# Performance work log

Measured on AMD Instinct MI355X. Metric: run time of the kernel, lower is better.

Reference implementation:

```python
import jax, jax.numpy as jnp
import numpy as np

# 2^22-point radix-2 DIT FFT; NOTE the original code applies tf.abs at EVERY
# recursion level (not just the top), so each butterfly stage is followed by a
# magnitude + recomplexification. We reproduce that exact (non-standard) math.
N = 1 << 22
STAGES = 22


def _bitrev_perm(n, bits):
    # vectorized bit-reversal permutation (the order induced by the even/odd
    # decimation inputs[0::2] / inputs[1::2] recursion)
    x = np.arange(n)
    r = np.zeros(n, dtype=np.int64)
    for b in range(bits):
        r = (r << 1) | ((x >> b) & 1)
    return r


_PERM = jnp.asarray(_bitrev_perm(N, STAGES))


def setup_inputs() -> dict:
    key = jax.random.key(0)
    x = jax.random.normal(key, (N,), dtype=jnp.float32)
    return {"x": x}


def reference(x):
    # base case of the recursion: length-1 leaves are the bit-reversed inputs
    y = x[_PERM].astype(jnp.complex64)
    for s in range(1, STAGES + 1):  # fixed log2(N) stages, not a data loop
        m = 1 << s                  # sub-FFT size at this stage
        yb = y.reshape(N // m, m)   # [num_blocks, m]
        e = yb[:, : m // 2]         # 'even' sub-results
        o = yb[:, m // 2:]          # 'odd'  sub-results
        # twiddles W(m, k) = exp(-2*pi*i*k/m)
        tw = jnp.exp(
            jnp.complex64(-2j * np.pi) * jnp.arange(m // 2, dtype=jnp.float32) / m
        ).astype(jnp.complex64)
        t = tw[None, :] * o
        # butterfly then tf.abs (applied at every level in the original)
        mag = jnp.abs(jnp.concatenate([e + t, e - t], axis=1)).reshape(N)
        y = mag.astype(jnp.complex64) if s < STAGES else mag
    return y  # float32 magnitudes, shape [N]
```

## Files before the change

### kernel.cpp

```cpp
#include <hip/hip_runtime.h>
#include <math.h>


#define NBITS 22
#define RSQ2 0.70710678118654752440f

__device__ __forceinline__ float hsqrt(float x) { return __builtin_amdgcn_sqrtf(x); }

__device__ __forceinline__ void bf(float& e, float& o, float c, float s) {
    float rp = fmaf(c, o, e);
    float rm = fmaf(-c, o, e);
    float im = s * o;
    float im2 = im * im;
    e = hsqrt(fmaf(rp, rp, im2));
    o = hsqrt(fmaf(rm, rm, im2));
}
__device__ __forceinline__ void bf0(float& e, float& o) {
    float a = e + o, b = e - o;
    e = fabsf(a); o = fabsf(b);
}
__device__ __forceinline__ void bfq(float& e, float& o) {
    float h = hsqrt(fmaf(e, e, o * o));
    e = h; o = h;
}

__device__ __forceinline__ void radix8f(float v[8], float c2, float s2) {
    float c1 = fmaf(-2.f * s2, s2, 1.f);
    float s1 = 2.f * s2 * c2;
    float c0 = fmaf(-2.f * s1, s1, 1.f);
    float s0 = 2.f * s1 * c1;
    bf(v[0], v[1], c0, s0); bf(v[2], v[3], c0, s0);
    bf(v[4], v[5], c0, s0); bf(v[6], v[7], c0, s0);
    bf(v[0], v[2], c1, s1); bf(v[4], v[6], c1, s1);
    bf(v[1], v[3], -s1, c1); bf(v[5], v[7], -s1, c1);
    bf(v[0], v[4], c2, s2);
    float u = RSQ2 * (c2 - s2), w = RSQ2 * (c2 + s2);
    bf(v[1], v[5], u, w);
    bf(v[2], v[6], -s2, c2);
    bf(v[3], v[7], -w, u);
}

__device__ __forceinline__ void radix8z(float v[8]) {
    bf0(v[0], v[1]); bf0(v[2], v[3]); bf0(v[4], v[5]); bf0(v[6], v[7]);
    bf0(v[0], v[2]); bf0(v[4], v[6]);
    bfq(v[1], v[3]); bfq(v[5], v[7]);
    bf0(v[0], v[4]);
    bf(v[1], v[5], RSQ2, RSQ2);
    bfq(v[2], v[6]);
    bf(v[3], v[7], -RSQ2, RSQ2);
}

#define PAD32(i) ((i) + (((i) >> 5) << 2))

__global__ __launch_bounds__(256, 8) void fft_perm(const float* __restrict__ x,
                                                   float* __restrict__ y) {
    __shared__ float lds[64 * 65];
    const unsigned tid = threadIdx.x;
    const unsigned tx = tid & 63, g = tid >> 6;
    const unsigned C0 = (blockIdx.x & 31) * 64;
    const unsigned B0 = (blockIdx.x >> 5) * 64;

#pragma unroll
    for (int k = 0; k < 16; ++k) {
        unsigned r = g * 16 + k;
        unsigned a = __brev(C0 + r) >> (32 - 11);
        lds[r * 65 + tx] = x[a * 2048u + B0 + tx];
    }
    __syncthreads();

    float v[8];
#pragma unroll
    for (int q = 0; q < 2; ++q) {
        unsigned task = tid + 256u * q;
        unsigned c = task >> 3, grp = task & 7;
#pragma unroll
        for (int j = 0; j < 8; ++j) v[j] = lds[(grp * 8 + j) * 65 + c];
        radix8z(v);
        unsigned pr = __brev(B0 + c) >> (32 - 11);
        float* dst = y + pr * 2048u + C0 + grp * 8;
        *(float4*)(dst)     = make_float4(v[0], v[1], v[2], v[3]);
        *(float4*)(dst + 4) = make_float4(v[4], v[5], v[6], v[7]);
    }
}

__global__ __launch_bounds__(1024, 8) void fft_low(float* __restrict__ y) {
    __shared__ float lds[9216];
    const unsigned t = threadIdx.x;
    const unsigned base = blockIdx.x * 8192;
    float v[8];

    {
        const float4* src = (const float4*)(y + base + t * 8);
        float4 u0 = src[0], u1 = src[1];
        float* dst = &lds[PAD32(t * 8)];
        ((float4*)dst)[0] = u0;
        ((float4*)dst)[1] = u1;
    }
    __syncthreads();

    {
        const unsigned lo = t & 7, hi = t >> 3;
        const unsigned i0 = hi * 64 + lo;
#pragma unroll
        for (int j = 0; j < 8; ++j) v[j] = lds[PAD32(i0 + j * 8)];
        float r = (float)lo * (1.f / 64);
        radix8f(v, __builtin_amdgcn_cosf(r), __builtin_amdgcn_sinf(r));
#pragma unroll
        for (int j = 0; j < 8; ++j) lds[PAD32(i0 + j * 8)] = v[j];
    }
    __syncthreads();

    {
        const unsigned lo = t & 63, hi = t >> 6;
        const unsigned i0 = hi * 512 + lo;
#pragma unroll
        for (int j = 0; j < 8; ++j) v[j] = lds[PAD32(i0 + j * 64)];
        float r = (float)lo * (1.f / 512);
        radix8f(v, __builtin_amdgcn_cosf(r), __builtin_amdgcn_sinf(r));
#pragma unroll
        for (int j = 0; j < 8; ++j) lds[PAD32(i0 + j * 64)] = v[j];
    }
    __syncthreads();

    {
        const unsigned lo = t & 511, hi = t >> 9;
        const unsigned i0 = hi * 4096 + lo;
#pragma unroll
        for (int j = 0; j < 8; ++j) v[j] = lds[PAD32(i0 + j * 512)];
        float r = (float)lo * (1.f / 4096);
        radix8f(v, __builtin_amdgcn_cosf(r), __builtin_amdgcn_sinf(r));
#pragma unroll
        for (int j = 0; j < 8; ++j) lds[PAD32(i0 + j * 512)] = v[j];
    }
    __syncthreads();

    {
        float c = __builtin_amdgcn_cosf((float)t * (1.f / 8192));
        float s = __builtin_amdgcn_sinf((float)t * (1.f / 8192));
#pragma unroll
        for (int it = 0; it < 4; ++it) {
            const unsigned i = it * 1024 + t;
            float e = lds[PAD32(i)];
            float o = lds[PAD32(i + 4096)];
            bf(e, o, c, s);
            y[base + i] = e;
            y[base + i + 4096] = o;
            float nc = RSQ2 * (c - s);
            s = RSQ2 * (c + s);
            c = nc;
        }
    }
}

__global__ __launch_bounds__(1024, 8) void fft_high(float* __restrict__ y) {
    __shared__ float lds[512 * 17 + 16];
    const unsigned tt = threadIdx.x;
    const unsigned li = tt & 15, u = tt >> 4;
    const unsigned low = blockIdx.x * 16 + li;
    float v[8];

#pragma unroll
    for (int j = 0; j < 8; ++j) v[j] = y[low + 8192u * (u * 8 + j)];
    {
        float r = (float)low * (1.f / 65536);
        radix8f(v, __builtin_amdgcn_cosf(r), __builtin_amdgcn_sinf(r));
    }
#pragma unroll
    for (int j = 0; j < 8; ++j) lds[(u * 8 + j) * 17 + li] = v[j];
    __syncthreads();

    {
        const unsigned lo8 = u & 7, hi = u >> 3;
        const unsigned t0 = hi * 64 + lo8;
#pragma unroll
        for (int j = 0; j < 8; ++j) v[j] = lds[(t0 + j * 8) * 17 + li];
        float r = ((float)low + 8192.f * (float)lo8) * (1.f / 524288);
        radix8f(v, __builtin_amdgcn_cosf(r), __builtin_amdgcn_sinf(r));
#pragma unroll
        for (int j = 0; j < 8; ++j) lds[(t0 + j * 8) * 17 + li] = v[j];
    }
    __syncthreads();

    {
#pragma unroll
        for (int j = 0; j < 8; ++j) v[j] = lds[(u + j * 64) * 17 + li];
        float r = ((float)low + 8192.f * (float)u) * (1.f / 4194304);
        radix8f(v, __builtin_amdgcn_cosf(r), __builtin_amdgcn_sinf(r));
#pragma unroll
        for (int j = 0; j < 8; ++j) y[low + 8192u * (u + j * 64)] = v[j];
    }
}

extern "C" void kernel_launch(void* const* d_in, const int* in_sizes, int n_in,
                              void* d_out, int out_size, void* d_ws, size_t ws_size,
                              hipStream_t stream) {
    const float* x = (const float*)d_in[0];
    float* out = (float*)d_out;

    fft_perm<<<dim3(1024), dim3(256), 0, stream>>>(x, out);
    fft_low<<<dim3(512), dim3(1024), 0, stream>>>(out);
    fft_high<<<dim3(512), dim3(1024), 0, stream>>>(out);
}
```

Baseline: 103.4 us.

## Switch low/high FFT kernels to radix-32 per thread with fewer LDS passes

Replaces the three radix-8 LDS passes plus a final radix-2 in fft_low with two radix-32 passes, loading directly from global memory into registers. fft_high becomes a radix-32 then radix-16 pair instead of three radix-8 passes. A generic radixN template derives twiddles from constant-memory tables. The aim is fewer LDS round trips and barriers. In exchange, blocks shrink to 256 threads and each thread holds 32 live values, which raises register pressure and may reduce occupancy. The first fft_low load is strided rather than vectorised.

```diff
diff --git a/kernel.cpp b/kernel.cpp
--- a/kernel.cpp
+++ b/kernel.cpp
@@ -24,20 +24,37 @@
     e = h; o = h;
 }
 
-__device__ __forceinline__ void radix8f(float v[8], float c2, float s2) {
-    float c1 = fmaf(-2.f * s2, s2, 1.f);
-    float s1 = 2.f * s2 * c2;
-    float c0 = fmaf(-2.f * s1, s1, 1.f);
-    float s0 = 2.f * s1 * c1;
-    bf(v[0], v[1], c0, s0); bf(v[2], v[3], c0, s0);
-    bf(v[4], v[5], c0, s0); bf(v[6], v[7], c0, s0);
-    bf(v[0], v[2], c1, s1); bf(v[4], v[6], c1, s1);
-    bf(v[1], v[3], -s1, c1); bf(v[5], v[7], -s1, c1);
-    bf(v[0], v[4], c2, s2);
-    float u = RSQ2 * (c2 - s2), w = RSQ2 * (c2 + s2);
-    bf(v[1], v[5], u, w);
-    bf(v[2], v[6], -s2, c2);
-    bf(v[3], v[7], -w, u);
+__device__ __constant__ float KC[16] = {
+    1.f, 0.980785280f, 0.923879533f, 0.831469612f, 0.707106781f, 0.555570233f,
+    0.382683432f, 0.195090322f, 0.f, -0.195090322f, -0.382683432f, -0.555570233f,
+    -0.707106781f, -0.831469612f, -0.923879533f, -0.980785280f };
+__device__ __constant__ float KS[16] = {
+    0.f, 0.195090322f, 0.382683432f, 0.555570233f, 0.707106781f, 0.831469612f,
+    0.923879533f, 0.980785280f, 1.f, 0.980785280f, 0.923879533f, 0.831469612f,
+    0.707106781f, 0.555570233f, 0.382683432f, 0.195090322f };
+
+template <int L>
+__device__ __forceinline__ void radixN(float* v, float c, float s) {
+    float ca[L], sa[L];
+    ca[L - 1] = c; sa[L - 1] = s;
+#pragma unroll
+    for (int a = L - 1; a > 0; --a) {
+        ca[a - 1] = fmaf(-2.f * sa[a], sa[a], 1.f);
+        sa[a - 1] = 2.f * sa[a] * ca[a];
+    }
+#pragma unroll
+    for (int a = 0; a < L; ++a) {
+        const int half = 1 << a;
+#pragma unroll
+        for (int d = 0; d < half; ++d) {
+            const int k = d << (4 - a);
+            float cd = fmaf(ca[a], KC[k], -sa[a] * KS[k]);
+            float sd = fmaf(sa[a], KC[k],  ca[a] * KS[k]);
+#pragma unroll
+            for (int g = d; g < (1 << L); g += 2 * half)
+                bf(v[g], v[g + half], cd, sd);
+        }
+    }
 }
 
 __device__ __forceinline__ void radix8z(float v[8]) {
@@ -49,8 +66,6 @@
     bfq(v[2], v[6]);
     bf(v[3], v[7], -RSQ2, RSQ2);
 }
-
-#define PAD32(i) ((i) + (((i) >> 5) << 2))
 
 __global__ __launch_bounds__(256, 8) void fft_perm(const float* __restrict__ x,
                                                    float* __restrict__ y) {
@@ -83,111 +98,76 @@
     }
 }
 
-__global__ __launch_bounds__(1024, 8) void fft_low(float* __restrict__ y) {
-    __shared__ float lds[9216];
+__global__ __launch_bounds__(256, 4) void fft_low(float* __restrict__ y) {
+    __shared__ float lds[8448];
     const unsigned t = threadIdx.x;
     const unsigned base = blockIdx.x * 8192;
-    float v[8];
+    const unsigned lo = t & 7, hi = t >> 3;
+    float v[32];
 
     {
-        const float4* src = (const float4*)(y + base + t * 8);
-        float4 u0 = src[0], u1 = src[1];
-        float* dst = &lds[PAD32(t * 8)];
-        ((float4*)dst)[0] = u0;
-        ((float4*)dst)[1] = u1;
-    }
-    __syncthreads();
-
-    {
-        const unsigned lo = t & 7, hi = t >> 3;
-        const unsigned i0 = hi * 64 + lo;
+        const float* src = y + base + lo + 256u * hi;
 #pragma unroll
-        for (int j = 0; j < 8; ++j) v[j] = lds[PAD32(i0 + j * 8)];
-        float r = (float)lo * (1.f / 64);
-        radix8f(v, __builtin_amdgcn_cosf(r), __builtin_amdgcn_sinf(r));
+        for (int j = 0; j < 32; ++j) v[j] = src[8 * j];
+        float r = (float)lo * (1.f / 256.f);
+        radixN<5>(v, __builtin_amdgcn_cosf(r), __builtin_amdgcn_sinf(r));
 #pragma unroll
-        for (int j = 0; j < 8; ++j) lds[PAD32(i0 + j * 8)] = v[j];
-    }
-    __syncthreads();
-
-    {
-        const unsigned lo = t & 63, hi = t >> 6;
-        const unsigned i0 = hi * 512 + lo;
-#pragma unroll
-        for (int j = 0; j < 8; ++j) v[j] = lds[PAD32(i0 + j * 64)];
-        float r = (float)lo * (1.f / 512);
-        radix8f(v, __builtin_amdgcn_cosf(r), __builtin_amdgcn_sinf(r));
-#pragma unroll
-        for (int j = 0; j < 8; ++j) lds[PAD32(i0 + j * 64)] = v[j];
-    }
-    __syncthreads();
-
-    {
-        const unsigned lo = t & 511, hi = t >> 9;
-        const unsigned i0 = hi * 4096 + lo;
-#pragma unroll
-        for (int j = 0; j < 8; ++j) v[j] = lds[PAD32(i0 + j * 512)];
-        float r = (float)lo * (1.f / 4096);
-        radix8f(v, __builtin_amdgcn_cosf(r), __builtin_amdgcn_sinf(r));
-#pragma unroll
-        for (int j = 0; j < 8; ++j) lds[PAD32(i0 + j * 512)] = v[j];
-    }
-    __syncthreads();
-
-    {
-        float c = __builtin_amdgcn_cosf((float)t * (1.f / 8192));
-        float s = __builtin_amdgcn_sinf((float)t * (1.f / 8192));
-#pragma unroll
-        for (int it = 0; it < 4; ++it) {
-            const unsigned i = it * 1024 + t;
-            float e = lds[PAD32(i)];
-            float o = lds[PAD32(i + 4096)];
-            bf(e, o, c, s);
-            y[base + i] = e;
-            y[base + i + 4096] = o;
-            float nc = RSQ2 * (c - s);
-            s = RSQ2 * (c + s);
-            c = nc;
+        for (int j = 0; j < 32; ++j) {
+            unsigned q = lo + 8u * j + 256u * hi;
+            lds[q + (q >> 5)] = v[j];
         }
-    }
-}
-
-__global__ __launch_bounds__(1024, 8) void fft_high(float* __restrict__ y) {
-    __shared__ float lds[512 * 17 + 16];
-    const unsigned tt = threadIdx.x;
-    const unsigned li = tt & 15, u = tt >> 4;
-    const unsigned low = blockIdx.x * 16 + li;
-    float v[8];
-
-#pragma unroll
-    for (int j = 0; j < 8; ++j) v[j] = y[low + 8192u * (u * 8 + j)];
-    {
-        float r = (float)low * (1.f / 65536);
-        radix8f(v, __builtin_amdgcn_cosf(r), __builtin_amdgcn_sinf(r));
-    }
-#pragma unroll
-    for (int j = 0; j < 8; ++j) lds[(u * 8 + j) * 17 + li] = v[j];
-    __syncthreads();
-
-    {
-        const unsigned lo8 = u & 7, hi = u >> 3;
-        const unsigned t0 = hi * 64 + lo8;
-#pragma unroll
-        for (int j = 0; j < 8; ++j) v[j] = lds[(t0 + j * 8) * 17 + li];
-        float r = ((float)low + 8192.f * (float)lo8) * (1.f / 524288);
-        radix8f(v, __builtin_amdgcn_cosf(r), __builtin_amdgcn_sinf(r));
-#pragma unroll
-        for (int j = 0; j < 8; ++j) lds[(t0 + j * 8) * 17 + li] = v[j];
     }
     __syncthreads();
 
     {
 #pragma unroll
-        for (int j = 0; j < 8; ++j) v[j] = lds[(u + j * 64) * 17 + li];
-        float r = ((float)low + 8192.f * (float)u) * (1.f / 4194304);
-        radix8f(v, __builtin_amdgcn_cosf(r), __builtin_amdgcn_sinf(r));
+        for (int j = 0; j < 32; ++j) {
+            unsigned q = t + 256u * j;
+            v[j] = lds[q + (q >> 5)];
+        }
+        float r = (float)t * (1.f / 8192.f);
+        radixN<5>(v, __builtin_amdgcn_cosf(r), __builtin_amdgcn_sinf(r));
+        float* dst = y + base + t;
 #pragma unroll
-        for (int j = 0; j < 8; ++j) y[low + 8192u * (u + j * 64)] = v[j];
+        for (int j = 0; j < 32; ++j) dst[256u * j] = v[j];
+    }
+}
+
+__global__ __launch_bounds__(256, 4) void fft_high(float* __restrict__ y) {
+    __shared__ float lds[512 * 17 + 32];
+    const unsigned tt = threadIdx.x;
+    const unsigned li = tt & 15, u5 = tt >> 4;
+    const unsigned low = blockIdx.x * 16 + li;
+    float v[32];
+
+    {
+        const float* src = y + low;
+#pragma unroll
+        for (int j = 0; j < 32; ++j) v[j] = src[8192u * (32u * u5 + j)];
+        float r = (float)low * (1.f / 262144.f);
+        radixN<5>(v, __builtin_amdgcn_cosf(r), __builtin_amdgcn_sinf(r));
+#pragma unroll
+        for (int j = 0; j < 32; ++j) {
+            unsigned trow = 32u * u5 + j;
+            lds[trow * 17 + (trow >> 5) + li] = v[j];
+        }
+    }
+    __syncthreads();
+
+#pragma unroll
+    for (int b = 0; b < 2; ++b) {
+        const unsigned t0 = 2u * u5 + b;
+        float* w = v + 16 * b;
+#pragma unroll
+        for (int j = 0; j < 16; ++j) {
+            unsigned trow = t0 + 32u * j;
+            w[j] = lds[trow * 17 + (trow >> 5) + li];
+        }
+        float r = ((float)low + 8192.f * (float)t0) * (1.f / 4194304.f);
+        radixN<4>(w, __builtin_amdgcn_cosf(r), __builtin_amdgcn_sinf(r));
+#pragma unroll
+        for (int j = 0; j < 16; ++j)
+            y[low + 8192u * (t0 + 32u * j)] = w[j];
     }
 }
 
@@ -198,6 +178,6 @@
     float* out = (float*)d_out;
 
     fft_perm<<<dim3(1024), dim3(256), 0, stream>>>(x, out);
-    fft_low<<<dim3(512), dim3(1024), 0, stream>>>(out);
-    fft_high<<<dim3(512), dim3(1024), 0, stream>>>(out);
+    fft_low<<<dim3(512), dim3(256), 0, stream>>>(out);
+    fft_high<<<dim3(512), dim3(256), 0, stream>>>(out);
 }
```

Result: faster. 100.6 us (median of 2 runs) (-2.8%).
